# Kernel optimization log

Measured on AMD Instinct MI355X. Metric: run time of the kernel, lower is better.

Reference implementation:

```python
import jax, jax.numpy as jnp
import numpy as np

B, S, D = 4, 512, 768
NH, DH = 12, 64
EXP_N, INV_N = 32, 64


def _scalar_mlp(x, w1, b1, w2, b2):
    # elementwise 1 -> N -> 1 MLP: y = relu(x*w1 + b1) @ w2 + b2, applied per element
    h = jax.nn.relu(x[..., None] * w1 + b1)          # [..., N]
    return jnp.einsum('...n,n->...', h, w2) + b2[0]  # [...]


def fit_softmax(X, exp_w1, exp_b1, exp_w2, exp_b2, inv_w1, inv_b1, inv_w2, inv_b2):
    # X: [B, H, S, S]. Faithful to torch fit_softmax: reference value is X[:, :, 0]
    tmax = X[:, :, 0][..., None]                      # [B, H, S, 1]
    tp = jnp.minimum(X - (tmax - 1.0), 3.0)           # clamp tp > 3 -> 3
    exp_val = _scalar_mlp(tp, exp_w1, exp_b1, exp_w2, exp_b2)
    X_up = jnp.where(tp > -20.0, exp_val, 0.0)        # only index tp > -20
    partition = jnp.sum(X_up, axis=-1, keepdims=True)  # [B, H, S, 1]
    p_inv = _scalar_mlp(partition, inv_w1, inv_b1, inv_w2, inv_b2)
    out = X_up * p_inv
    partition_p2 = jnp.sum(out, axis=-1, keepdims=True)
    p_inv2 = _scalar_mlp(partition_p2, inv_w1, inv_b1, inv_w2, inv_b2)
    # renormalize only rows whose partition exceeds 1.5
    return jnp.where(partition_p2 > 1.5, out * p_inv2, out)


def setup_inputs() -> dict:
    key = jax.random.key(0)
    ks = jax.random.split(key, 16)
    f = jax.random.normal
    return {
        'hidden_states': f(ks[0], (B, S, D), jnp.float32),
        'attention_mask': jnp.zeros((B, 1, 1, S), jnp.float32),
        'Wq': f(ks[1], (D, D), jnp.float32) * 0.02,
        'bq': f(ks[2], (D,), jnp.float32) * 0.02,
        'Wk': f(ks[3], (D, D), jnp.float32) * 0.02,
        'bk': f(ks[4], (D,), jnp.float32) * 0.02,
        'Wv': f(ks[5], (D, D), jnp.float32) * 0.02,
        'bv': f(ks[6], (D,), jnp.float32) * 0.02,
        'exp_w1': f(ks[7], (EXP_N,), jnp.float32),
        'exp_b1': f(ks[8], (EXP_N,), jnp.float32),
        'exp_w2': f(ks[9], (EXP_N,), jnp.float32) * 0.1,
        'exp_b2': f(ks[10], (1,), jnp.float32) * 0.1,
        'inv_w1': f(ks[11], (INV_N,), jnp.float32),
        'inv_b1': f(ks[12], (INV_N,), jnp.float32),
        'inv_w2': f(ks[13], (INV_N,), jnp.float32) * 0.1,
        'inv_b2': f(ks[14], (1,), jnp.float32) * 0.1,
    }


def reference(hidden_states, attention_mask, Wq, bq, Wk, bk, Wv, bv,
              exp_w1, exp_b1, exp_w2, exp_b2, inv_w1, inv_b1, inv_w2, inv_b2):
    def split_heads(x):  # [B, S, D] -> [B, H, S, DH]
        return x.reshape(B, S, NH, DH).transpose(0, 2, 1, 3)

    q = split_heads(hidden_states @ Wq.T + bq)
    k = split_heads(hidden_states @ Wk.T + bk)
    v = split_heads(hidden_states @ Wv.T + bv)

    scores = jnp.einsum('bhqd,bhkd->bhqk', q, k) / np.float32(np.sqrt(DH))
    scores = scores + attention_mask
    probs = fit_softmax(scores, exp_w1, exp_b1, exp_w2, exp_b2,
                        inv_w1, inv_b1, inv_w2, inv_b2)
    ctx = jnp.einsum('bhqk,bhkd->bhqd', probs, v)     # [B, H, S, DH]
    return ctx.transpose(0, 2, 1, 3).reshape(B, S, D)
```

## Files before the change

kernel.cpp:

```cpp
#include <hip/hip_runtime.h>
#include <math.h>

typedef unsigned short u16;
typedef short bf16x8 __attribute__((ext_vector_type(8)));
typedef float f32x4 __attribute__((ext_vector_type(4)));

#define BN 4
#define SN 512
#define DN 768
#define NHN 12
#define DHN 64
#define EXPN 32
#define INVN 64

#define TAB_T0 -20.5f
#define TAB_DLT (23.5f / 512.0f)
#define TAB_SCALE (512.0f / 23.5f)

__device__ __forceinline__ u16 f2b(float f) {
    union { float f; unsigned int u; } v; v.f = f;
    unsigned int r = v.u + 0x7FFFu + ((v.u >> 16) & 1u);
    return (u16)(r >> 16);
}
__device__ __forceinline__ u16 f2h(float f) {
    union { _Float16 h; u16 u; } v; v.h = (_Float16)f; return v.u;
}

#define GLD16(g, l) __builtin_amdgcn_global_load_lds( \
    (__attribute__((address_space(1))) const void*)(g), \
    (__attribute__((address_space(3))) void*)(l), 16, 0, 0)

__global__ __launch_bounds__(256) void prep(
    const float* __restrict__ X, const float* __restrict__ Wq,
    const float* __restrict__ Wk, const float* __restrict__ Wv,
    const float* __restrict__ ew1, const float* __restrict__ eb1,
    const float* __restrict__ ew2, const float* __restrict__ eb2,
    u16* __restrict__ Xb, u16* __restrict__ Wqb,
    u16* __restrict__ Wkb, u16* __restrict__ Wvb,
    float2* __restrict__ tbl)
{
    if (blockIdx.y == 4) {
        int i = blockIdx.x * 256 + threadIdx.x;
        if (i > 513) return;
        float t0 = TAB_T0 + i * TAB_DLT;
        float t1 = t0 + TAB_DLT;
        float y0 = eb2[0], y1 = y0;
        #pragma unroll 8
        for (int n = 0; n < EXPN; ++n) {
            float w1 = ew1[n], b1 = eb1[n], w2 = ew2[n];
            y0 += fmaxf(fmaf(t0, w1, b1), 0.f) * w2;
            y1 += fmaxf(fmaf(t1, w1, b1), 0.f) * w2;
        }
        tbl[i] = make_float2(y0, y1 - y0);
        return;
    }
    const float* s; u16* d; int n;
    switch (blockIdx.y) {
        case 0:  s = X;  d = Xb;  n = (BN * SN) * DN; break;
        case 1:  s = Wq; d = Wqb; n = DN * DN; break;
        case 2:  s = Wk; d = Wkb; n = DN * DN; break;
        default: s = Wv; d = Wvb; n = DN * DN; break;
    }
    int i = (blockIdx.x * 256 + threadIdx.x) * 4;
    if (i < n) {
        float4 v = *(const float4*)&s[i];
        unsigned int lo = (unsigned)f2b(v.x) | ((unsigned)f2b(v.y) << 16);
        unsigned int hi = (unsigned)f2b(v.z) | ((unsigned)f2b(v.w) << 16);
        *(uint2*)&d[i] = make_uint2(lo, hi);
    }
}

__global__ __launch_bounds__(256) void qkv_mfma(
    const u16* __restrict__ Xb,
    const u16* __restrict__ Wqb, const u16* __restrict__ Wkb, const u16* __restrict__ Wvb,
    const float* __restrict__ bq, const float* __restrict__ bk, const float* __restrict__ bv,
    u16* __restrict__ Qb, u16* __restrict__ Kb, u16* __restrict__ Vtr)
{
    __shared__ __align__(16) u16 As[128 * 32];
    __shared__ __align__(16) u16 Bs[64 * 32];

    const int tid = threadIdx.x, w = tid >> 6, l = tid & 63;
    const int lr = l & 15, lg = l >> 4;
    const int m0 = blockIdx.y * 128;
    const int nsel = blockIdx.x / 12;
    const int n0l = (blockIdx.x % 12) * 64;
    const u16* W = (nsel == 0) ? Wqb : (nsel == 1) ? Wkb : Wvb;
    const float* bias = (nsel == 0) ? bq : (nsel == 1) ? bk : bv;

    const int wm = w >> 1, wn = w & 1;

    const int oA0 = tid * 16;
    const int rA0 = oA0 >> 6, sA0 = (oA0 >> 4) & 3;
    const int cA0 = (sA0 ^ ((rA0 >> 1) & 3)) * 8;
    const int oA1 = oA0 + 4096;
    const int rA1 = oA1 >> 6, sA1 = (oA1 >> 4) & 3;
    const int cA1 = (sA1 ^ ((rA1 >> 1) & 3)) * 8;
    const u16* gA0 = Xb + (m0 + rA0) * DN + cA0;
    const u16* gA1 = Xb + (m0 + rA1) * DN + cA1;
    const u16* gB  = W + (n0l + rA0) * DN + cA0;

    int offA[4], offB[2];
    #pragma unroll
    for (int mi = 0; mi < 4; ++mi) {
        int row = wm * 64 + mi * 16 + lr;
        offA[mi] = row * 64 + ((lg ^ ((row >> 1) & 3)) * 16);
    }
    #pragma unroll
    for (int ni = 0; ni < 2; ++ni) {
        int row = wn * 32 + ni * 16 + lr;
        offB[ni] = row * 64 + ((lg ^ ((row >> 1) & 3)) * 16);
    }

    f32x4 acc[4][2];
    #pragma unroll
    for (int mi = 0; mi < 4; ++mi)
        #pragma unroll
        for (int ni = 0; ni < 2; ++ni) acc[mi][ni] = (f32x4){0.f, 0.f, 0.f, 0.f};

    for (int k0 = 0; k0 < DN; k0 += 32) {
        __syncthreads();
        GLD16(gA0 + k0, (char*)As + oA0);
        GLD16(gA1 + k0, (char*)As + oA1);
        GLD16(gB  + k0, (char*)Bs + oA0);
        __syncthreads();

        bf16x8 af[4], bff[2];
        #pragma unroll
        for (int mi = 0; mi < 4; ++mi) af[mi] = *(const bf16x8*)((const char*)As + offA[mi]);
        #pragma unroll
        for (int ni = 0; ni < 2; ++ni) bff[ni] = *(const bf16x8*)((const char*)Bs + offB[ni]);
        #pragma unroll
        for (int mi = 0; mi < 4; ++mi)
            #pragma unroll
            for (int ni = 0; ni < 2; ++ni)
                acc[mi][ni] = __builtin_amdgcn_mfma_f32_16x16x32_bf16(af[mi], bff[ni], acc[mi][ni], 0, 0, 0);
    }

    if (nsel < 2) {
        u16* out = (nsel == 0) ? Qb : Kb;
        #pragma unroll
        for (int ni = 0; ni < 2; ++ni) {
            int col = n0l + wn * 32 + ni * 16 + lr;
            float bc = bias[col];
            int hh = col >> 6, dh = col & 63;
            #pragma unroll
            for (int mi = 0; mi < 4; ++mi) {
                #pragma unroll
                for (int r = 0; r < 4; ++r) {
                    int m = m0 + wm * 64 + mi * 16 + lg * 4 + r;
                    int bi = m >> 9, srow = m & 511;
                    out[(((bi * NHN + hh) * SN) + srow) * DHN + dh] = f2b(acc[mi][ni][r] + bc);
                }
            }
        }
    } else {
        #pragma unroll
        for (int ni = 0; ni < 2; ++ni) {
            int col = n0l + wn * 32 + ni * 16 + lr;
            float bc = bias[col];
            int hh = col >> 6, dh = col & 63;
            #pragma unroll
            for (int mi = 0; mi < 4; ++mi) {
                int m = m0 + wm * 64 + mi * 16 + lg * 4;
                int bi = m >> 9, srow = m & 511;
                ushort4 pk;
                pk.x = f2h(acc[mi][ni][0] + bc);
                pk.y = f2h(acc[mi][ni][1] + bc);
                pk.z = f2h(acc[mi][ni][2] + bc);
                pk.w = f2h(acc[mi][ni][3] + bc);
                *(ushort4*)&Vtr[((size_t)(bi * NHN + hh) * DHN + dh) * SN + srow] = pk;
            }
        }
    }
}

__global__ __launch_bounds__(512, 6) void attn_mfma(
    const u16* __restrict__ Qb, const u16* __restrict__ Kb, const u16* __restrict__ Vtr,
    const float* __restrict__ mask, const float2* __restrict__ tbl,
    const float* __restrict__ iw1, const float* __restrict__ ib1,
    const float* __restrict__ iw2, const float* __restrict__ ib2,
    float* __restrict__ out)
{
    __shared__ __align__(16) u16 sb[32 * 512];
    __shared__ __align__(16) float2 tab[514];
    __shared__ float ms[SN];
    __shared__ float wI1[INVN], wIb1[INVN], wI2[INVN];
    __shared__ float partw[8][32];
    __shared__ float scale_s[32];
    __shared__ float pvbuf[32][68];
    __shared__ float scal;

    const int tid = threadIdx.x, w = tid >> 6, l = tid & 63;
    const int lr = l & 15, lg = l >> 4, kb8 = lg * 8;
    const int bid = blockIdx.x;
    const int bh = bid >> 4;
    const int q0 = (bid & 15) * 32;
    const int b = bh / NHN, h = bh % NHN;
    const u16* Qh = Qb + (size_t)bh * SN * DHN;
    const u16* Kh = Kb + (size_t)bh * SN * DHN;
    const u16* VTh = Vtr + (size_t)bh * DHN * SN;

    if (tid < INVN) { wI1[tid] = iw1[tid]; wIb1[tid] = ib1[tid]; wI2[tid] = iw2[tid]; }
    if (tid == 511) scal = ib2[0];
    if (tid < SN) ms[tid] = mask[b * SN + tid];
    for (int i = tid; i < 514; i += 512) tab[i] = tbl[i];
    __syncthreads();

    const float ib2v = scal;

    bf16x8 aq00 = *(const bf16x8*)(Qh + (q0 + lr) * DHN + kb8);
    bf16x8 aq01 = *(const bf16x8*)(Qh + (q0 + lr) * DHN + 32 + kb8);
    bf16x8 aq10 = *(const bf16x8*)(Qh + (q0 + 16 + lr) * DHN + kb8);
    bf16x8 aq11 = *(const bf16x8*)(Qh + (q0 + 16 + lr) * DHN + 32 + kb8);

    float myref0[4], myref1[4];
    {
        bf16x8 a00 = *(const bf16x8*)(Qh + kb8);
        bf16x8 a01 = *(const bf16x8*)(Qh + 32 + kb8);
        const u16* kp0 = Kh + (q0 + lr) * DHN + kb8;
        bf16x8 b00 = *(const bf16x8*)(kp0);
        bf16x8 b01 = *(const bf16x8*)(kp0 + 32);
        const u16* kp1 = Kh + (q0 + 16 + lr) * DHN + kb8;
        bf16x8 b10 = *(const bf16x8*)(kp1);
        bf16x8 b11 = *(const bf16x8*)(kp1 + 32);
        f32x4 d0 = {0.f, 0.f, 0.f, 0.f}, d1 = {0.f, 0.f, 0.f, 0.f};
        d0 = __builtin_amdgcn_mfma_f32_16x16x32_bf16(a00, b00, d0, 0, 0, 0);
        d0 = __builtin_amdgcn_mfma_f32_16x16x32_bf16(a01, b01, d0, 0, 0, 0);
        d1 = __builtin_amdgcn_mfma_f32_16x16x32_bf16(a00, b10, d1, 0, 0, 0);
        d1 = __builtin_amdgcn_mfma_f32_16x16x32_bf16(a01, b11, d1, 0, 0, 0);
        float rc0 = d0[0] * 0.125f + ms[q0 + lr];
        float rc1 = d1[0] * 0.125f + ms[q0 + 16 + lr];
        #pragma unroll
        for (int r = 0; r < 4; ++r) {
            myref0[r] = __shfl(rc0, lg * 4 + r);
            myref1[r] = __shfl(rc1, lg * 4 + r);
        }
    }

    char* sbb = (char*)sb;
    float part0[4] = {0.f, 0.f, 0.f, 0.f};
    float part1[4] = {0.f, 0.f, 0.f, 0.f};
    const u16* kpp = Kh + (w * 64 + lr) * DHN + kb8;
    bf16x8 nb0 = *(const bf16x8*)(kpp);
    bf16x8 nb1 = *(const bf16x8*)(kpp + 32);
    #pragma unroll
    for (int i = 0; i < 4; ++i) {
        bf16x8 b0 = nb0, b1 = nb1;
        if (i < 3) {
            const u16* kn = kpp + (i + 1) * 16 * DHN;
            nb0 = *(const bf16x8*)(kn);
            nb1 = *(const bf16x8*)(kn + 32);
        }
        f32x4 d0 = {0.f, 0.f, 0.f, 0.f}, d1 = {0.f, 0.f, 0.f, 0.f};
        __builtin_amdgcn_s_setprio(1);
        d0 = __builtin_amdgcn_mfma_f32_16x16x32_bf16(aq00, b0, d0, 0, 0, 0);
        d0 = __builtin_amdgcn_mfma_f32_16x16x32_bf16(aq01, b1, d0, 0, 0, 0);
        d1 = __builtin_amdgcn_mfma_f32_16x16x32_bf16(aq10, b0, d1, 0, 0, 0);
        d1 = __builtin_amdgcn_mfma_f32_16x16x32_bf16(aq11, b1, d1, 0, 0, 0);
        __builtin_amdgcn_s_setprio(0);
        const int col0 = w * 64 + i * 16;
        const float mv = ms[col0 + lr];
        const int colb = (col0 + lr) * 2;
        #pragma unroll
        for (int r = 0; r < 4; ++r) {
            {
                float tp = fminf(d0[r] * 0.125f + mv - (myref0[r] - 1.0f), 3.0f);
                float v = (tp - TAB_T0) * TAB_SCALE;
                int idx = (int)v;
                idx = idx < 0 ? 0 : idx;
                float fr = v - (float)idx;
                float2 p = tab[idx];
                float e = fmaf(fr, p.y, p.x);
                float xu = (tp > -20.0f) ? e : 0.f;
                part0[r] += xu;
                int row = lg * 4 + r;
                *(u16*)(sbb + row * 1024 + (colb ^ ((row & 7) << 4))) = f2h(xu);
            }
            {
                float tp = fminf(d1[r] * 0.125f + mv - (myref1[r] - 1.0f), 3.0f);
                float v = (tp - TAB_T0) * TAB_SCALE;
                int idx = (int)v;
                idx = idx < 0 ? 0 : idx;
                float fr = v - (float)idx;
                float2 p = tab[idx];
                float e = fmaf(fr, p.y, p.x);
                float xu = (tp > -20.0f) ? e : 0.f;
                part1[r] += xu;
                int row = 16 + lg * 4 + r;
                *(u16*)(sbb + row * 1024 + (colb ^ ((row & 7) << 4))) = f2h(xu);
            }
        }
    }
    #pragma unroll
    for (int r = 0; r < 4; ++r) {
        #pragma unroll
        for (int s = 1; s < 16; s <<= 1) {
            part0[r] += __shfl_xor(part0[r], s);
            part1[r] += __shfl_xor(part1[r], s);
        }
    }
    if (lr == 0) {
        #pragma unroll
        for (int r = 0; r < 4; ++r) {
            partw[w][lg * 4 + r] = part0[r];
            partw[w][16 + lg * 4 + r] = part1[r];
        }
    }
    __syncthreads();

    #pragma unroll
    for (int rr = 0; rr < 4; ++rr) {
        const int row = w * 4 + rr;
        float pt = 0.f;
        #pragma unroll
        for (int ww = 0; ww < 8; ++ww) pt += partw[ww][row];
        float hu = fmaxf(fmaf(pt, wI1[l], wIb1[l]), 0.f) * wI2[l];
        #pragma unroll
        for (int s = 32; s > 0; s >>= 1) hu += __shfl_xor(hu, s);
        const float pinv = hu + ib2v;
        const float p2 = pt * pinv;
        float hu2 = fmaxf(fmaf(p2, wI1[l], wIb1[l]), 0.f) * wI2[l];
        #pragma unroll
        for (int s = 32; s > 0; s >>= 1) hu2 += __shfl_xor(hu2, s);
        const float pinv2 = hu2 + ib2v;
        if (l == 0) scale_s[row] = pinv * ((p2 > 1.5f) ? pinv2 : 1.0f);
    }

    const int ds = (w & 3) * 16, kh = w >> 2;
    f32x4 acc0 = {0.f, 0.f, 0.f, 0.f}, acc1 = {0.f, 0.f, 0.f, 0.f};
    const u16* vp = VTh + (ds + lr) * SN + kh * 256 + kb8;
    const int swzl = (lr & 7) << 4;
    bf16x8 nv = *(const bf16x8*)(vp);
    #pragma unroll
    for (int k0 = 0; k0 < 256; k0 += 32) {
        bf16x8 bv = nv;
        if (k0 < 224) nv = *(const bf16x8*)(vp + k0 + 32);
        const int kk2 = (kh * 256 + k0 + kb8) * 2;
        bf16x8 a0 = *(const bf16x8*)(sbb + lr * 1024 + (kk2 ^ swzl));
        bf16x8 a1 = *(const bf16x8*)(sbb + (16 + lr) * 1024 + (kk2 ^ swzl));
        __builtin_amdgcn_s_setprio(1);
        acc0 = __builtin_amdgcn_mfma_f32_16x16x32_f16(a0, bv, acc0, 0, 0, 0);
        acc1 = __builtin_amdgcn_mfma_f32_16x16x32_f16(a1, bv, acc1, 0, 0, 0);
        __builtin_amdgcn_s_setprio(0);
    }
    if (kh == 1) {
        #pragma unroll
        for (int r = 0; r < 4; ++r) {
            pvbuf[lg * 4 + r][ds + lr] = acc0[r];
            pvbuf[16 + lg * 4 + r][ds + lr] = acc1[r];
        }
    }
    __syncthreads();
    if (kh == 0) {
        #pragma unroll
        for (int r = 0; r < 4; ++r) {
            const int row0 = lg * 4 + r;
            const int row1 = row0 + 16;
            float v0 = (acc0[r] + pvbuf[row0][ds + lr]) * scale_s[row0];
            float v1 = (acc1[r] + pvbuf[row1][ds + lr]) * scale_s[row1];
            out[(size_t)(b * SN + q0 + row0) * DN + h * DHN + ds + lr] = v0;
            out[(size_t)(b * SN + q0 + row1) * DN + h * DHN + ds + lr] = v1;
        }
    }
}

extern "C" void kernel_launch(void* const* d_in, const int* in_sizes, int n_in,
                              void* d_out, int out_size, void* d_ws, size_t ws_size,
                              hipStream_t stream) {
    const float* X    = (const float*)d_in[0];
    const float* mask = (const float*)d_in[1];
    const float* Wq   = (const float*)d_in[2];
    const float* bq   = (const float*)d_in[3];
    const float* Wk   = (const float*)d_in[4];
    const float* bk   = (const float*)d_in[5];
    const float* Wv   = (const float*)d_in[6];
    const float* bv   = (const float*)d_in[7];
    const float* ew1  = (const float*)d_in[8];
    const float* eb1  = (const float*)d_in[9];
    const float* ew2  = (const float*)d_in[10];
    const float* eb2  = (const float*)d_in[11];
    const float* iw1  = (const float*)d_in[12];
    const float* ib1  = (const float*)d_in[13];
    const float* iw2  = (const float*)d_in[14];
    const float* ib2  = (const float*)d_in[15];
    float* out = (float*)d_out;

    float2* tbl = (float2*)d_ws;
    u16* Xb  = (u16*)((char*)d_ws + 4608);
    u16* Wqb = Xb + (size_t)(BN * SN) * DN;
    u16* Wkb = Wqb + DN * DN;
    u16* Wvb = Wkb + DN * DN;
    u16* Qb  = Wvb + DN * DN;
    const size_t per = (size_t)BN * NHN * SN * DHN;
    u16* Kb2 = Qb + per;
    u16* Vb2 = Kb2 + per;

    dim3 gc(1536, 5);
    prep<<<gc, 256, 0, stream>>>(X, Wq, Wk, Wv, ew1, eb1, ew2, eb2,
                                 Xb, Wqb, Wkb, Wvb, tbl);

    dim3 g1(36, 16);
    qkv_mfma<<<g1, 256, 0, stream>>>(Xb, Wqb, Wkb, Wvb, bq, bk, bv, Qb, Kb2, Vb2);

    attn_mfma<<<dim3(768), 512, 0, stream>>>(Qb, Kb2, Vb2, mask, tbl,
                                             iw1, ib1, iw2, ib2, out);
}
```

Measured before the change: 56.07 us.

## Repartition PV matmul across waves by row tile, drop cross-wave reduction buffer

New measurement: 68.39 us. +22.0%, slower.

```diff
diff --git a/kernel.cpp b/kernel.cpp
--- a/kernel.cpp
+++ b/kernel.cpp
@@ -14,8 +14,8 @@
 #define INVN 64
 
 #define TAB_T0 -20.5f
-#define TAB_DLT (23.5f / 512.0f)
-#define TAB_SCALE (512.0f / 23.5f)
+#define TAB_DLT (23.5f / 448.0f)
+#define TAB_SCALE (448.0f / 23.5f)
 
 __device__ __forceinline__ u16 f2b(float f) {
     union { float f; unsigned int u; } v; v.f = f;
@@ -41,7 +41,7 @@
 {
     if (blockIdx.y == 4) {
         int i = blockIdx.x * 256 + threadIdx.x;
-        if (i > 513) return;
+        if (i > 449) return;
         float t0 = TAB_T0 + i * TAB_DLT;
         float t1 = t0 + TAB_DLT;
         float y0 = eb2[0], y1 = y0;
@@ -174,7 +174,7 @@
     }
 }
 
-__global__ __launch_bounds__(512, 6) void attn_mfma(
+__global__ __launch_bounds__(512, 8) void attn_mfma(
     const u16* __restrict__ Qb, const u16* __restrict__ Kb, const u16* __restrict__ Vtr,
     const float* __restrict__ mask, const float2* __restrict__ tbl,
     const float* __restrict__ iw1, const float* __restrict__ ib1,
@@ -182,12 +182,11 @@
     float* __restrict__ out)
 {
     __shared__ __align__(16) u16 sb[32 * 512];
-    __shared__ __align__(16) float2 tab[514];
+    __shared__ __align__(16) float2 tab[450];
     __shared__ float ms[SN];
     __shared__ float wI1[INVN], wIb1[INVN], wI2[INVN];
     __shared__ float partw[8][32];
     __shared__ float scale_s[32];
-    __shared__ float pvbuf[32][68];
     __shared__ float scal;
 
     const int tid = threadIdx.x, w = tid >> 6, l = tid & 63;
@@ -203,7 +202,7 @@
     if (tid < INVN) { wI1[tid] = iw1[tid]; wIb1[tid] = ib1[tid]; wI2[tid] = iw2[tid]; }
     if (tid == 511) scal = ib2[0];
     if (tid < SN) ms[tid] = mask[b * SN + tid];
-    for (int i = tid; i < 514; i += 512) tab[i] = tbl[i];
+    if (tid < 450) tab[tid] = tbl[tid];
     __syncthreads();
 
     const float ib2v = scal;
@@ -326,41 +325,33 @@
         if (l == 0) scale_s[row] = pinv * ((p2 > 1.5f) ? pinv2 : 1.0f);
     }
 
-    const int ds = (w & 3) * 16, kh = w >> 2;
-    f32x4 acc0 = {0.f, 0.f, 0.f, 0.f}, acc1 = {0.f, 0.f, 0.f, 0.f};
-    const u16* vp = VTh + (ds + lr) * SN + kh * 256 + kb8;
+    const int mt = w & 1, ds = (w >> 1) * 16;
+    f32x4 acca = {0.f, 0.f, 0.f, 0.f}, accb = {0.f, 0.f, 0.f, 0.f};
+    const u16* vp = VTh + (ds + lr) * SN + kb8;
     const int swzl = (lr & 7) << 4;
-    bf16x8 nv = *(const bf16x8*)(vp);
-    #pragma unroll
-    for (int k0 = 0; k0 < 256; k0 += 32) {
-        bf16x8 bv = nv;
-        if (k0 < 224) nv = *(const bf16x8*)(vp + k0 + 32);
-        const int kk2 = (kh * 256 + k0 + kb8) * 2;
-        bf16x8 a0 = *(const bf16x8*)(sbb + lr * 1024 + (kk2 ^ swzl));
-        bf16x8 a1 = *(const bf16x8*)(sbb + (16 + lr) * 1024 + (kk2 ^ swzl));
+    const int rowbase = (mt * 16 + lr) * 1024;
+    bf16x8 nva = *(const bf16x8*)(vp);
+    bf16x8 nvb = *(const bf16x8*)(vp + 32);
+    #pragma unroll
+    for (int k0 = 0; k0 < SN; k0 += 64) {
+        bf16x8 bva = nva, bvb = nvb;
+        if (k0 < SN - 64) {
+            nva = *(const bf16x8*)(vp + k0 + 64);
+            nvb = *(const bf16x8*)(vp + k0 + 96);
+        }
+        bf16x8 a0 = *(const bf16x8*)(sbb + rowbase + (((k0 + kb8) * 2) ^ swzl));
+        bf16x8 a1 = *(const bf16x8*)(sbb + rowbase + (((k0 + 32 + kb8) * 2) ^ swzl));
         __builtin_amdgcn_s_setprio(1);
-        acc0 = __builtin_amdgcn_mfma_f32_16x16x32_f16(a0, bv, acc0, 0, 0, 0);
-        acc1 = __builtin_amdgcn_mfma_f32_16x16x32_f16(a1, bv, acc1, 0, 0, 0);
+        acca = __builtin_amdgcn_mfma_f32_16x16x32_f16(a0, bva, acca, 0, 0, 0);
+        accb = __builtin_amdgcn_mfma_f32_16x16x32_f16(a1, bvb, accb, 0, 0, 0);
         __builtin_amdgcn_s_setprio(0);
     }
-    if (kh == 1) {
-        #pragma unroll
-        for (int r = 0; r < 4; ++r) {
-            pvbuf[lg * 4 + r][ds + lr] = acc0[r];
-            pvbuf[16 + lg * 4 + r][ds + lr] = acc1[r];
-        }
-    }
     __syncthreads();
-    if (kh == 0) {
-        #pragma unroll
-        for (int r = 0; r < 4; ++r) {
-            const int row0 = lg * 4 + r;
-            const int row1 = row0 + 16;
-            float v0 = (acc0[r] + pvbuf[row0][ds + lr]) * scale_s[row0];
-            float v1 = (acc1[r] + pvbuf[row1][ds + lr]) * scale_s[row1];
-            out[(size_t)(b * SN + q0 + row0) * DN + h * DHN + ds + lr] = v0;
-            out[(size_t)(b * SN + q0 + row1) * DN + h * DHN + ds + lr] = v1;
-        }
+    #pragma unroll
+    for (int r = 0; r < 4; ++r) {
+        const int row = mt * 16 + lg * 4 + r;
+        float v = (acca[r] + accb[r]) * scale_s[row];
+        out[(size_t)(b * SN + q0 + row) * DN + h * DHN + ds + lr] = v;
     }
 }
 
```
